# Kernel tuning notes

Hardware: AMD Instinct MI355X
Metric: run time of the kernel (lower is better)

Reference implementation:

```python
import jax, jax.numpy as jnp
import numpy as np

K = 1023   # kernel_size == embedding_dim
H = 16     # out_channels (filters per sample)
E = 256    # num_embeddings
T = 8      # num_tokens
CC = 0.25  # commitment cost
EPS = np.float32(np.finfo(np.float32).eps)
DN = ('NCH', 'OIH', 'NCH')


def setup_inputs() -> dict:
    key = jax.random.key(0)
    ks = jax.random.split(key, 10)
    B, C, L = 8, 1, 8184
    D_ff = 2 * E
    X = jax.random.normal(ks[0], (B, C, L), jnp.float32)
    embedding = jax.random.uniform(ks[1], (E, K), jnp.float32, -1.0 / E, 1.0 / E)
    ffn_w1 = jax.random.normal(ks[2], (E, D_ff), jnp.float32) * 0.02
    ffn_b1 = jnp.zeros((D_ff,), jnp.float32)
    ffn_w2 = jax.random.normal(ks[3], (D_ff, E), jnp.float32) * 0.02
    ffn_b2 = jnp.zeros((E,), jnp.float32)
    ln_g = jnp.ones((E,), jnp.float32)
    ln_b = jnp.zeros((E,), jnp.float32)
    cls_w = jax.random.normal(ks[4], (E, 10), jnp.float32) * 0.02
    cls_b = jnp.zeros((10,), jnp.float32)
    return dict(X=X, embedding=embedding, ffn_w1=ffn_w1, ffn_b1=ffn_b1,
                ffn_w2=ffn_w2, ffn_b2=ffn_b2, ln_g=ln_g, ln_b=ln_b,
                cls_w=cls_w, cls_b=cls_b)


def _autocov(f):
    # f: [..., K]. FFT-based autocovariance of hann-windowed, max-normalized frame.
    n = f.shape[-1]
    fmax = jnp.max(jnp.abs(f), axis=-1, keepdims=True)
    fmax = jnp.where(fmax == 0, EPS, fmax)
    win = 0.5 * (1.0 - jnp.cos(2.0 * jnp.pi * jnp.arange(n, dtype=jnp.float32) / n))
    xw = f * win / fmax
    spec = jnp.abs(jnp.fft.rfft(xw, n=n) ** 2)   # |rfft(x)^2| == |rfft(x)|^2
    return jnp.fft.ifftshift(jnp.fft.irfft(spec, n=n), axes=-1)


def reference(X, embedding, ffn_w1, ffn_b1, ffn_w2, ffn_b2, ln_g, ln_b, cls_w, cls_b):
    B, C, L = X.shape
    # ---- encoder: extract frames at fixed linspace positions, autocovariance ----
    Lp = ((L + K - 1) // K) * K          # PadForConv(zero) length (no-op here)
    end = Lp - K - 1 - K
    positions = jnp.linspace(0.0, float(end), H).astype(jnp.int32)
    idx = positions[:, None] + jnp.arange(K)          # (H, K)
    frames = X[:, :, idx]                             # (B, C, H, K) gather
    Z = _autocov(jnp.transpose(frames, (0, 2, 1, 3)))  # (B, H, C, K)
    # ---- VQ: pairwise distances + argmin + codebook lookup ----
    flat = Z.reshape(-1, K)                           # (B*H*C, K)
    d = (jnp.sum(flat ** 2, axis=1, keepdims=True)
         + jnp.sum(embedding ** 2, axis=1)
         - 2.0 * flat @ embedding.T)                  # (B*H*C, E)
    codes = jnp.argmin(d, axis=1)
    enc = jax.nn.one_hot(codes, E, dtype=flat.dtype)
    quant = (enc @ embedding).reshape(Z.shape)
    sg = jax.lax.stop_gradient
    e_loss = jnp.mean((sg(quant) - Z) ** 2)
    q_loss = jnp.mean((quant - sg(Z)) ** 2)
    vq_loss = q_loss + CC * e_loss
    quant_st = Z + sg(quant - Z)                      # straight-through
    avg = jnp.mean(enc, axis=0)
    perplexity = jnp.exp(-jnp.sum(avg * jnp.log(avg + EPS)))
    # ---- decoder: every sample's filter bank convolved with the whole batch ----
    fmerged = quant_st.reshape(B * H, C, K)           # merge per-sample banks
    out = jax.lax.conv_general_dilated(X, fmerged, (1,), 'SAME',
                                       dimension_numbers=DN)  # (B, B*H, L)
    out = out.reshape(B, B, H, L)                     # (batch b, filter-sample i, k, L)
    sq = (out - X[:, None, :, :]) ** 2                # C==1 broadcast
    # sum_i mean_k mse_{b,l} == mean over (b,k,l) then sum over i
    recon_loss = jnp.sum(jnp.mean(sq, axis=(0, 2, 3)))
    # ---- project: conv with codebook as filters ----
    pfilt = jnp.broadcast_to(embedding[:, None, :], (E, C, K))
    proj = jax.lax.conv_general_dilated(X, pfilt, (1,), 'VALID',
                                        dimension_numbers=DN)  # (B, E, Lo)
    Lo = proj.shape[-1]
    pad = ((Lo + T - 1) // T) * T - Lo                # PadForConv(mean)
    m = jnp.mean(proj, axis=-1, keepdims=True)
    proj = jnp.concatenate([proj, jnp.broadcast_to(m, (B, E, pad))], axis=-1)
    # ---- classify ----
    x = proj.reshape(B, E, T, -1).transpose(0, 2, 3, 1)  # (B, T, t, E)
    x = jnp.max(x, axis=2)                               # (B, T, E)
    mu = jnp.mean(x, axis=-1, keepdims=True)
    var = jnp.var(x, axis=-1, keepdims=True)
    xn = (x - mu) / jnp.sqrt(var + 1e-5) * ln_g + ln_b
    hdd = jax.nn.relu(xn @ ffn_w1 + ffn_b1) @ ffn_w2 + ffn_b2
    feat = jnp.mean(hdd, axis=1)                         # (B, E)
    logits = feat @ cls_w + cls_b
    return (logits, vq_loss, recon_loss, perplexity)
```

## Files before the change

### kernel.cpp

```cpp
#include <hip/hip_runtime.h>

#define KK 1023
#define LL 8184
#define LO 7162
#define XPS 10240
#define EPSF 1.1920928955078125e-07f
#define NEG_INF (-3.4028234663852886e+38f)

typedef short bf16x8 __attribute__((ext_vector_type(8)));
typedef float f32x4 __attribute__((ext_vector_type(4)));

__device__ __constant__ int c_pos[16] = {0,409,818,1227,1636,2045,2454,2863,
                                         3273,3682,4091,4500,4909,5318,5727,6137};

__device__ __forceinline__ unsigned short f2bf(float f) {
    unsigned u = __float_as_uint(f);
    unsigned r = (u + 0x7FFFu + ((u >> 16) & 1u)) >> 16;
    return (unsigned short)r;
}
__device__ __forceinline__ int fenc(float f) {
    int u = __float_as_int(f);
    return u >= 0 ? u : (~u) ^ 0x80000000;
}
__device__ __forceinline__ float fdec(int k) {
    int u = k >= 0 ? k : ~(k ^ 0x80000000);
    return __int_as_float(u);
}
__device__ __forceinline__ void gl2lds16(const void* g, void* l) {
    __builtin_amdgcn_global_load_lds(
        (const __attribute__((address_space(1))) void*)g,
        (__attribute__((address_space(3))) void*)l, 16, 0, 0);
}

__global__ __launch_bounds__(256) void k_pa(const float* __restrict__ X,
                                            const float* __restrict__ emb,
                                            unsigned short* __restrict__ Xpad,
                                            unsigned short* __restrict__ Xodd,
                                            unsigned short* __restrict__ Ebf,
                                            float* __restrict__ Etf,
                                            float* __restrict__ enorm,
                                            int* __restrict__ hist,
                                            int* __restrict__ cmax,
                                            float* __restrict__ Z) {
    __shared__ __align__(16) float xw[2048];
    __shared__ float red[256];
    const int q = blockIdx.x;
    const int tid = threadIdx.x;
    if (q < 256) {
        const int fi = q >> 1, half = q & 1;
        const int b = fi >> 4, h = fi & 15;
        const float* xp = X + b * LL + c_pos[h];
        float lmax = 0.f;
        for (int j = tid; j < KK; j += 256) {
            float v = xp[j];
            xw[j] = v;
            lmax = fmaxf(lmax, fabsf(v));
        }
        red[tid] = lmax;
        __syncthreads();
        for (int off = 128; off; off >>= 1) {
            if (tid < off) red[tid] = fmaxf(red[tid], red[tid + off]);
            __syncthreads();
        }
        float fmx = red[0];
        if (fmx == 0.f) fmx = EPSF;
        __syncthreads();
        for (int j = tid; j < KK; j += 256) {
            float v = xw[j];
            float win = 0.5f * (1.0f - cosf(6.28318530717958647692f * (float)j / 1023.0f));
            float w = v * win / fmx;
            xw[j] = w;
            xw[j + KK] = w;
        }
        __syncthreads();

        if (tid < 128) {
            const int m = half * 512 + 4 * tid;
            const int mh = m >> 1;
            const int mq4 = mh >> 1;
            const float2* X2 = (const float2*)xw;
            const float4* X4 = (const float4*)xw;
            float a0 = 0.f, a1 = 0.f, a2 = 0.f, a3 = 0.f;
            float2 W0 = X2[mh], W1 = X2[mh + 1], W2 = X2[mh + 2], W3 = X2[mh + 3];
            for (int jh = 0; jh < 510; jh += 2) {
                float4 nw = X4[mq4 + (jh >> 1) + 2];
                float4 xj = X4[jh >> 1];
                a0 = fmaf(xj.x, W0.x, a0);
                a0 = fmaf(xj.y, W0.y, a0);
                a0 = fmaf(xj.z, W1.x, a0);
                a0 = fmaf(xj.w, W1.y, a0);
                a1 = fmaf(xj.x, W0.y, a1);
                a1 = fmaf(xj.y, W1.x, a1);
                a1 = fmaf(xj.z, W1.y, a1);
                a1 = fmaf(xj.w, W2.x, a1);
                a2 = fmaf(xj.x, W1.x, a2);
                a2 = fmaf(xj.y, W1.y, a2);
                a2 = fmaf(xj.z, W2.x, a2);
                a2 = fmaf(xj.w, W2.y, a2);
                a3 = fmaf(xj.x, W1.y, a3);
                a3 = fmaf(xj.y, W2.x, a3);
                a3 = fmaf(xj.z, W2.y, a3);
                a3 = fmaf(xj.w, W3.x, a3);
                W0 = W2; W1 = W3;
                W2 = make_float2(nw.x, nw.y);
                W3 = make_float2(nw.z, nw.w);
            }
            {
                float2 xj = X2[510];
                a0 = fmaf(xj.x, W0.x, a0);
                a0 = fmaf(xj.y, W0.y, a0);
                a1 = fmaf(xj.x, W0.y, a1);
                a1 = fmaf(xj.y, W1.x, a1);
                a2 = fmaf(xj.x, W1.x, a2);
                a2 = fmaf(xj.y, W1.y, a2);
                a3 = fmaf(xj.x, W1.y, a3);
                a3 = fmaf(xj.y, W2.x, a3);
            }
            float xt = xw[1022];
            a0 = fmaf(xt, W1.x, a0);
            a1 = fmaf(xt, W1.y, a1);
            a2 = fmaf(xt, W2.x, a2);
            a3 = fmaf(xt, W2.y, a3);

            float* zrow = Z + fi * KK;
            float av[4] = {a0, a1, a2, a3};
#pragma unroll
            for (int qq = 0; qq < 4; ++qq) {
                int mmq = m + qq;
                if (mmq < KK) {
                    int i0 = mmq + 512; if (i0 >= KK) i0 -= KK;
                    zrow[i0] = av[qq];
                }
            }
        }
    } else if (q < 288) {
        const int qq = q - 256;
        const int b = qq >> 2, seg = qq & 3;
        for (int i = seg * 2560 + tid; i < (seg + 1) * 2560; i += 256) {
            unsigned short v = 0, vo = 0;
            if (i >= 512 && i < 512 + LL) v = f2bf(X[b * LL + (i - 512)]);
            const int i1 = i + 1;
            if (i1 >= 512 && i1 < 512 + LL) vo = f2bf(X[b * LL + (i1 - 512)]);
            Xpad[b * XPS + i] = v;
            Xodd[b * XPS + i] = vo;
        }
    } else if (q < 544) {
        const int e = q - 288;
        const float* er = emb + e * KK;
        float nrm = 0.f;
        for (int k = tid; k < 1024; k += 256) {
            float v = (k < KK) ? er[k] : 0.f;
            Ebf[e * 1024 + k] = (k < KK) ? f2bf(v) : (unsigned short)0;
            Etf[(k >> 2) * 1024 + e * 4 + (k & 3)] = v;
            nrm = fmaf(v, v, nrm);
        }
        red[tid] = nrm;
        __syncthreads();
        for (int off = 128; off; off >>= 1) {
            if (tid < off) red[tid] += red[tid + off];
            __syncthreads();
        }
        if (tid == 0) enorm[e] = red[0];
    } else {
        const int i = (q - 544) * 256 + tid;
        cmax[i] = INT_MIN;
        if (q == 544) hist[tid] = 0;
    }
}

__global__ __launch_bounds__(256) void k_vq(const float* __restrict__ Z,
                                            const float4* __restrict__ Et4,
                                            const float* __restrict__ enorm,
                                            const float* __restrict__ emb,
                                            int* __restrict__ codes,
                                            int* __restrict__ hist,
                                            float* __restrict__ vq_part) {
    __shared__ float zl[KK];
    __shared__ __align__(16) float zm2[1024];
    __shared__ float rv[256];
    __shared__ int   ri[256];
    const int fi = blockIdx.x, tid = threadIdx.x;
    const float* zrow = Z + fi * KK;
    for (int t = tid; t < 1024; t += 256) {
        float z = (t < KK) ? zrow[t] : 0.f;
        if (t < KK) zl[t] = z;
        zm2[t] = -2.f * z;
    }
    __syncthreads();

    float d = enorm[tid];
    const float4* zp = (const float4*)zm2;
    const float4* ep = Et4 + tid;
#pragma unroll 8
    for (int t4 = 0; t4 < 256; ++t4) {
        float4 ev = ep[t4 * 256];
        float4 zv = zp[t4];
        d = fmaf(zv.x, ev.x, d);
        d = fmaf(zv.y, ev.y, d);
        d = fmaf(zv.z, ev.z, d);
        d = fmaf(zv.w, ev.w, d);
    }
    rv[tid] = d; ri[tid] = tid;
    __syncthreads();
    for (int off = 128; off; off >>= 1) {
        if (tid < off) {
            float v2 = rv[tid + off]; int i2 = ri[tid + off];
            if (v2 < rv[tid] || (v2 == rv[tid] && i2 < ri[tid])) { rv[tid] = v2; ri[tid] = i2; }
        }
        __syncthreads();
    }
    const int code = ri[0];
    if (tid == 0) { codes[fi] = code; atomicAdd(&hist[code], 1); }

    const float* qr = emb + code * KK;
    float s = 0.f;
    for (int t = tid; t < KK; t += 256) { float dd = qr[t] - zl[t]; s += dd * dd; }
    __syncthreads();
    rv[tid] = s;
    __syncthreads();
    for (int off = 128; off; off >>= 1) {
        if (tid < off) rv[tid] += rv[tid + off];
        __syncthreads();
    }
    if (tid == 0) vq_part[fi] = rv[0];
}

__global__ __launch_bounds__(256, 4) void k_gemm(const unsigned short* __restrict__ Xpad,
                                                 const unsigned short* __restrict__ Xodd,
                                                 const unsigned short* __restrict__ Ebf,
                                                 const int* __restrict__ codes,
                                                 const float* __restrict__ X,
                                                 float* __restrict__ psum_part,
                                                 float* __restrict__ recon_part,
                                                 int* __restrict__ cmax) {
    __shared__ __align__(16) unsigned short lds_b[8 * 1280];
    __shared__ __align__(16) unsigned short lds_a[2 * 2048];
    __shared__ float red_s[64][4];
    const int tid  = threadIdx.x;
    const int lane = tid & 63;
    const int c = lane & 15, g = lane >> 4;
    const int wg = tid >> 6;

    const int bi = blockIdx.x;
    const bool isproj = bi < 896;
    int b, l0, row0;
    if (isproj) { b = bi / 112; int r = bi % 112; row0 = (r / 28) * 64; l0 = (r % 28) * 256; }
    else        { int q = bi - 896; b = q >> 6; int r = q & 63; row0 = (r >> 5) * 64; l0 = (r & 31) * 256; }
    const int xw0 = (isproj ? 512 : 0) + l0;

    {
        const unsigned short* base_e = Xpad + b * XPS + xw0;
        const unsigned short* base_o = Xodd + b * XPS + xw0;
        for (int k = tid; k < 1280; k += 256) {
            const int wdw = k / 160;
            const int p = k - wdw * 160;
            const unsigned short* src = (wdw & 1) ? (base_o + wdw - 1 + p * 8)
                                                  : (base_e + wdw + p * 8);
            gl2lds16(src, lds_b + k * 8);
        }
    }
    const int r_lds = tid >> 2, q4 = tid & 3;
    const int grow = isproj ? (row0 + r_lds) : codes[row0 + r_lds];
    const unsigned short* e_src = Ebf + grow * 1024 + q4 * 8;
    gl2lds16(e_src, lds_a + tid * 8);
    __syncthreads();

    f32x4 acc[4][4];
#pragma unroll
    for (int i = 0; i < 4; ++i)
#pragma unroll
        for (int j = 0; j < 4; ++j) acc[i][j] = (f32x4){0.f, 0.f, 0.f, 0.f};

    const char* lax = (const char*)lds_a;
    const char* lbx = (const char*)lds_b;
    const int boff0 = (wg & 1) * 10240 + ((wg >> 1) << 4) + 32 * c + 16 * g;
    const int aoff0 = c * 64 + g * 16;

    for (int s = 0; s < 32; ++s) {
        const int cur = s & 1;
        if (s + 1 < 32)
            gl2lds16(e_src + (s + 1) * 32, lds_a + ((s + 1) & 1) * 2048 + tid * 8);
        const char* ab = lax + cur * 4096 + aoff0;
        bf16x8 af[4];
#pragma unroll
        for (int et = 0; et < 4; ++et) af[et] = *(const bf16x8*)(ab + et * 1024);
#pragma unroll
        for (int ntl = 0; ntl < 4; ++ntl) {
            bf16x8 bfrag = *(const bf16x8*)(lbx + boff0 + ntl * 2560 + 64 * s);
#pragma unroll
            for (int et = 0; et < 4; ++et)
                acc[et][ntl] = __builtin_amdgcn_mfma_f32_16x16x32_bf16(af[et], bfrag, acc[et][ntl], 0, 0, 0);
        }
        __syncthreads();
    }

    const int lseg  = l0 >> 8;
    const int lbase = l0 + wg * 4;
    if (isproj) {
        const int ch0 = lbase / 896;
#pragma unroll
        for (int et = 0; et < 4; ++et) {
#pragma unroll
            for (int r = 0; r < 4; ++r) {
                float ssum = 0.f, m0 = NEG_INF, m1 = NEG_INF;
#pragma unroll
                for (int ntl = 0; ntl < 4; ++ntl) {
                    float v = acc[et][ntl][r];
                    int l = lbase + ntl + 16 * c;
                    bool ok = l < LO;
                    ssum += ok ? v : 0.f;
                    int ch = l / 896;
                    if (ok && ch == ch0) m0 = fmaxf(m0, v);
                    if (ok && ch != ch0) m1 = fmaxf(m1, v);
                }
                ssum += __shfl_xor(ssum, 1); ssum += __shfl_xor(ssum, 2);
                ssum += __shfl_xor(ssum, 4); ssum += __shfl_xor(ssum, 8);
                m0 = fmaxf(m0, __shfl_xor(m0, 1)); m0 = fmaxf(m0, __shfl_xor(m0, 2));
                m0 = fmaxf(m0, __shfl_xor(m0, 4)); m0 = fmaxf(m0, __shfl_xor(m0, 8));
                m1 = fmaxf(m1, __shfl_xor(m1, 1)); m1 = fmaxf(m1, __shfl_xor(m1, 2));
                m1 = fmaxf(m1, __shfl_xor(m1, 4)); m1 = fmaxf(m1, __shfl_xor(m1, 8));
                if (c == 0) {
                    int eidx = et * 16 + g * 4 + r;
                    red_s[eidx][wg] = ssum;
                    int e = row0 + eidx;
                    int cb = (b * 256 + e) * 8;
                    if (m0 > NEG_INF && ch0 < 8)     atomicMax(&cmax[cb + ch0], fenc(m0));
                    if (m1 > NEG_INF && ch0 + 1 < 8) atomicMax(&cmax[cb + ch0 + 1], fenc(m1));
                }
            }
        }
    } else {
        float xv[4];
#pragma unroll
        for (int ntl = 0; ntl < 4; ++ntl) {
            int lr = lbase + ntl + 16 * c - 1;
            xv[ntl] = (lr >= 0 && lr < LL) ? X[b * LL + lr] : 0.f;
        }
#pragma unroll
        for (int et = 0; et < 4; ++et) {
#pragma unroll
            for (int r = 0; r < 4; ++r) {
                float ssum = 0.f;
#pragma unroll
                for (int ntl = 0; ntl < 4; ++ntl) {
                    int lr = lbase + ntl + 16 * c - 1;
                    bool ok = (lr >= 0) && (lr < LL);
                    float dd = ok ? (acc[et][ntl][r] - xv[ntl]) : 0.f;
                    ssum += dd * dd;
                }
                ssum += __shfl_xor(ssum, 1); ssum += __shfl_xor(ssum, 2);
                ssum += __shfl_xor(ssum, 4); ssum += __shfl_xor(ssum, 8);
                if (c == 0) red_s[et * 16 + g * 4 + r][wg] = ssum;
            }
        }
    }
    __syncthreads();
    if (tid < 64) {
        float tot = red_s[tid][0] + red_s[tid][1] + red_s[tid][2] + red_s[tid][3];
        if (isproj) {
            int e = row0 + tid;
            psum_part[lseg * 2048 + b * 256 + e] = tot;
        } else {
            int f = row0 + tid;
            recon_part[(b * 128 + f) * 32 + lseg] = tot;
        }
    }
}

__global__ __launch_bounds__(256) void k_lnffn1(const float* __restrict__ psum_part,
                                                const int* __restrict__ cmax,
                                                const float* __restrict__ ln_g,
                                                const float* __restrict__ ln_b,
                                                const float* __restrict__ w1,
                                                const float* __restrict__ b1,
                                                float* __restrict__ hbuf) {
    __shared__ float red[256];
    __shared__ float red2[256];
    __shared__ float xr[256];
    const int bt = blockIdx.x;
    const int t = bt & 7;
    const int b = bt >> 3;
    const int e = threadIdx.x;
    const float* ps = psum_part + b * 256 + e;
    float sm = 0.f;
#pragma unroll
    for (int s = 0; s < 28; ++s) sm += ps[s * 2048];
    float m = sm * (1.0f / 7162.0f);
    const int cb = (b * 256 + e) << 3;
    float v = (t < 7) ? fdec(cmax[cb + t]) : fmaxf(fdec(cmax[cb + 7]), m);
    red[e] = v; red2[e] = v * v;
    __syncthreads();
    for (int off = 128; off; off >>= 1) {
        if (e < off) { red[e] += red[e + off]; red2[e] += red2[e + off]; }
        __syncthreads();
    }
    float mu  = red[0] * (1.0f / 256.0f);
    float var = red2[0] * (1.0f / 256.0f) - mu * mu;
    float r = 1.0f / sqrtf(var + 1e-5f);
    xr[e] = (v - mu) * r * ln_g[e] + ln_b[e];
    __syncthreads();

    float a0 = 0.f, a1 = 0.f;
#pragma unroll 4
    for (int ee = 0; ee < 256; ++ee) {
        float xv = xr[ee];
        a0 = fmaf(xv, w1[ee * 512 + e], a0);
        a1 = fmaf(xv, w1[ee * 512 + 256 + e], a1);
    }
    hbuf[bt * 512 + e]       = fmaxf(a0 + b1[e], 0.f);
    hbuf[bt * 512 + 256 + e] = fmaxf(a1 + b1[256 + e], 0.f);
}

__global__ __launch_bounds__(256) void k_ffn2(const float* __restrict__ hbuf,
                                              const float* __restrict__ w2,
                                              const float* __restrict__ b2,
                                              float* __restrict__ hdd) {
    __shared__ float hr[512];
    __shared__ float rv[256];
    const int q = blockIdx.x;
    const int bt = q & 63, jc = q >> 6;
    const int tid = threadIdx.x;
    hr[tid] = hbuf[bt * 512 + tid];
    hr[tid + 256] = hbuf[bt * 512 + 256 + tid];
    __syncthreads();
    const int jj = tid & 63, ks = tid >> 6;
    const int e = jc * 64 + jj;
    const float* wp = w2 + (ks * 128) * 256 + e;
    float a = 0.f;
#pragma unroll
    for (int j = 0; j < 128; ++j) a = fmaf(hr[ks * 128 + j], wp[j * 256], a);
    rv[tid] = a;
    __syncthreads();
    if (tid < 64) {
        float s = rv[tid] + rv[tid + 64] + rv[tid + 128] + rv[tid + 192];
        hdd[bt * 256 + jc * 64 + tid] = s + b2[jc * 64 + tid];
    }
}

__global__ __launch_bounds__(256) void k_final(const float* __restrict__ hdd,
                                               const float* __restrict__ cls_w,
                                               const float* __restrict__ cls_b,
                                               const float* __restrict__ recon_part,
                                               const float* __restrict__ vq_part,
                                               const int* __restrict__ hist,
                                               float* __restrict__ out) {
    __shared__ float red[256];
    const int tid = threadIdx.x;
    if (blockIdx.x == 0) {
        __shared__ float feat[8][256];
#pragma unroll
        for (int b2 = 0; b2 < 8; ++b2) {
            float fb = 0.f;
#pragma unroll
            for (int t2 = 0; t2 < 8; ++t2) fb += hdd[(b2 * 8 + t2) * 256 + tid];
            feat[b2][tid] = fb * 0.125f;
        }
        __syncthreads();
        if (tid < 80) {
            const int b = tid / 10, k = tid % 10;
            float a = cls_b[k];
            for (int e = 0; e < 256; ++e) a = fmaf(feat[b][e], cls_w[e * 10 + k], a);
            out[tid] = a;
        }
    } else {
        float s = 0.f;
        for (int i = tid; i < 32768; i += 256) s += recon_part[i];
        red[tid] = s;
        __syncthreads();
        for (int off = 128; off; off >>= 1) { if (tid < off) red[tid] += red[tid + off]; __syncthreads(); }
        if (tid == 0) out[81] = red[0] / 1047552.0f;
        __syncthreads();
        red[tid] = (tid < 128) ? vq_part[tid] : 0.f;
        __syncthreads();
        for (int off = 128; off; off >>= 1) { if (tid < off) red[tid] += red[tid + off]; __syncthreads(); }
        if (tid == 0) out[80] = 1.25f * red[0] / 130944.0f;
        __syncthreads();
        float avg = (float)hist[tid] * (1.0f / 128.0f);
        red[tid] = avg * logf(avg + EPSF);
        __syncthreads();
        for (int off = 128; off; off >>= 1) { if (tid < off) red[tid] += red[tid + off]; __syncthreads(); }
        if (tid == 0) out[82] = expf(-red[0]);
    }
}

extern "C" void kernel_launch(void* const* d_in, const int* in_sizes, int n_in,
                              void* d_out, int out_size, void* d_ws, size_t ws_size,
                              hipStream_t stream) {
    const float* X     = (const float*)d_in[0];
    const float* emb   = (const float*)d_in[1];
    const float* w1    = (const float*)d_in[2];
    const float* b1    = (const float*)d_in[3];
    const float* w2    = (const float*)d_in[4];
    const float* b2    = (const float*)d_in[5];
    const float* ln_g  = (const float*)d_in[6];
    const float* ln_b  = (const float*)d_in[7];
    const float* cls_w = (const float*)d_in[8];
    const float* cls_b = (const float*)d_in[9];
    float* out = (float*)d_out;

    float* Z            = (float*)d_ws;
    float* vq_part      = Z + 130944;
    float* xnbuf        = vq_part + 128;
    float* hdd          = xnbuf + 16384;
    float* psum_part    = hdd + 16384;
    float* recon_part   = psum_part + 65536;
    int*   cmaxb        = (int*)(recon_part + 32768);
    int*   codes        = cmaxb + 16384;
    int*   hist         = codes + 128;
    unsigned short* Xpad = (unsigned short*)(hist + 256);
    unsigned short* Xodd = Xpad + 8 * XPS;
    unsigned short* Ebf  = Xodd + 8 * XPS;
    float* Etf           = (float*)(Ebf + 256 * 1024);
    float* enorm         = Etf + 256 * 1024;
    float* hbuf          = enorm + 256;

    k_pa     <<<dim3(608), dim3(256), 0, stream>>>(X, emb, Xpad, Xodd, Ebf, Etf, enorm, hist, cmaxb, Z);
    k_vq     <<<dim3(128), dim3(256), 0, stream>>>(Z, (const float4*)Etf, enorm, emb, codes, hist, vq_part);
    k_gemm   <<<dim3(1408), dim3(256), 0, stream>>>(Xpad, Xodd, Ebf, codes, X, psum_part, recon_part, cmaxb);
    k_lnffn1 <<<dim3(64),  dim3(256), 0, stream>>>(psum_part, cmaxb, ln_g, ln_b, w1, b1, hbuf);
    k_ffn2   <<<dim3(256), dim3(256), 0, stream>>>(hbuf, w2, b2, hdd);
    k_final  <<<dim3(2),   dim3(256), 0, stream>>>(hdd, cls_w, cls_b, recon_part, vq_part, hist, out);
}
```

Before: 139.9 us.

## Restructure kernel graph to overlap independent stages in merged launches

The VQ kernel is merged with the projection GEMM blocks, and the LayerNorm/FFN1 stage is merged with the reconstruction GEMM blocks. FFN2 is merged with the loss reductions, and the classifier becomes its own tiny kernel. Each launch now runs independent work side by side, which cuts serial dependency depth and fills idle CUs with small tail stages. The cost is shared-memory union sizing and branch-divergent block roles that may change occupancy.

```diff
diff --git a/kernel.cpp b/kernel.cpp
--- a/kernel.cpp
+++ b/kernel.cpp
@@ -168,85 +168,85 @@
     }
 }
 
-__global__ __launch_bounds__(256) void k_vq(const float* __restrict__ Z,
-                                            const float4* __restrict__ Et4,
-                                            const float* __restrict__ enorm,
-                                            const float* __restrict__ emb,
-                                            int* __restrict__ codes,
-                                            int* __restrict__ hist,
-                                            float* __restrict__ vq_part) {
-    __shared__ float zl[KK];
-    __shared__ __align__(16) float zm2[1024];
-    __shared__ float rv[256];
-    __shared__ int   ri[256];
-    const int fi = blockIdx.x, tid = threadIdx.x;
-    const float* zrow = Z + fi * KK;
-    for (int t = tid; t < 1024; t += 256) {
-        float z = (t < KK) ? zrow[t] : 0.f;
-        if (t < KK) zl[t] = z;
-        zm2[t] = -2.f * z;
-    }
-    __syncthreads();
-
-    float d = enorm[tid];
-    const float4* zp = (const float4*)zm2;
-    const float4* ep = Et4 + tid;
+__global__ __launch_bounds__(256, 4) void kA(const float* __restrict__ Z,
+                                             const float4* __restrict__ Et4,
+                                             const float* __restrict__ enorm,
+                                             const float* __restrict__ emb,
+                                             int* __restrict__ codes,
+                                             int* __restrict__ hist,
+                                             float* __restrict__ vq_part,
+                                             const unsigned short* __restrict__ Xpad,
+                                             const unsigned short* __restrict__ Xodd,
+                                             const unsigned short* __restrict__ Ebf,
+                                             float* __restrict__ psum_part,
+                                             int* __restrict__ cmax) {
+    __shared__ __align__(16) char smem[29696];
+    const int tid = threadIdx.x;
+    const int bi = blockIdx.x;
+    if (bi < 128) {
+        float* zl  = (float*)smem;
+        float* zm2 = (float*)(smem + 4096);
+        float* rv  = (float*)(smem + 8192);
+        int*   ri  = (int*)(smem + 9216);
+        const int fi = bi;
+        const float* zrow = Z + fi * KK;
+        for (int t = tid; t < 1024; t += 256) {
+            float z = (t < KK) ? zrow[t] : 0.f;
+            if (t < KK) zl[t] = z;
+            zm2[t] = -2.f * z;
+        }
+        __syncthreads();
+
+        float d = enorm[tid];
+        const float4* zp = (const float4*)zm2;
+        const float4* ep = Et4 + tid;
 #pragma unroll 8
-    for (int t4 = 0; t4 < 256; ++t4) {
-        float4 ev = ep[t4 * 256];
-        float4 zv = zp[t4];
-        d = fmaf(zv.x, ev.x, d);
-        d = fmaf(zv.y, ev.y, d);
-        d = fmaf(zv.z, ev.z, d);
-        d = fmaf(zv.w, ev.w, d);
-    }
-    rv[tid] = d; ri[tid] = tid;
-    __syncthreads();
-    for (int off = 128; off; off >>= 1) {
-        if (tid < off) {
-            float v2 = rv[tid + off]; int i2 = ri[tid + off];
-            if (v2 < rv[tid] || (v2 == rv[tid] && i2 < ri[tid])) { rv[tid] = v2; ri[tid] = i2; }
-        }
-        __syncthreads();
-    }
-    const int code = ri[0];
-    if (tid == 0) { codes[fi] = code; atomicAdd(&hist[code], 1); }
-
-    const float* qr = emb + code * KK;
-    float s = 0.f;
-    for (int t = tid; t < KK; t += 256) { float dd = qr[t] - zl[t]; s += dd * dd; }
-    __syncthreads();
-    rv[tid] = s;
-    __syncthreads();
-    for (int off = 128; off; off >>= 1) {
-        if (tid < off) rv[tid] += rv[tid + off];
-        __syncthreads();
-    }
-    if (tid == 0) vq_part[fi] = rv[0];
-}
-
-__global__ __launch_bounds__(256, 4) void k_gemm(const unsigned short* __restrict__ Xpad,
-                                                 const unsigned short* __restrict__ Xodd,
-                                                 const unsigned short* __restrict__ Ebf,
-                                                 const int* __restrict__ codes,
-                                                 const float* __restrict__ X,
-                                                 float* __restrict__ psum_part,
-                                                 float* __restrict__ recon_part,
-                                                 int* __restrict__ cmax) {
-    __shared__ __align__(16) unsigned short lds_b[8 * 1280];
-    __shared__ __align__(16) unsigned short lds_a[2 * 2048];
-    __shared__ float red_s[64][4];
-    const int tid  = threadIdx.x;
+        for (int t4 = 0; t4 < 256; ++t4) {
+            float4 ev = ep[t4 * 256];
+            float4 zv = zp[t4];
+            d = fmaf(zv.x, ev.x, d);
+            d = fmaf(zv.y, ev.y, d);
+            d = fmaf(zv.z, ev.z, d);
+            d = fmaf(zv.w, ev.w, d);
+        }
+        rv[tid] = d; ri[tid] = tid;
+        __syncthreads();
+        for (int off = 128; off; off >>= 1) {
+            if (tid < off) {
+                float v2 = rv[tid + off]; int i2 = ri[tid + off];
+                if (v2 < rv[tid] || (v2 == rv[tid] && i2 < ri[tid])) { rv[tid] = v2; ri[tid] = i2; }
+            }
+            __syncthreads();
+        }
+        const int code = ri[0];
+        if (tid == 0) { codes[fi] = code; atomicAdd(&hist[code], 1); }
+
+        const float* qr = emb + code * KK;
+        float s = 0.f;
+        for (int t = tid; t < KK; t += 256) { float dd = qr[t] - zl[t]; s += dd * dd; }
+        __syncthreads();
+        rv[tid] = s;
+        __syncthreads();
+        for (int off = 128; off; off >>= 1) {
+            if (tid < off) rv[tid] += rv[tid + off];
+            __syncthreads();
+        }
+        if (tid == 0) vq_part[fi] = rv[0];
+        return;
+    }
+    unsigned short* lds_b = (unsigned short*)smem;
+    unsigned short* lds_a = (unsigned short*)(smem + 20480);
+    float (*red_s)[4] = (float(*)[4])(smem + 28672);
     const int lane = tid & 63;
     const int c = lane & 15, g = lane >> 4;
     const int wg = tid >> 6;
 
-    const int bi = blockIdx.x;
-    const bool isproj = bi < 896;
-    int b, l0, row0;
-    if (isproj) { b = bi / 112; int r = bi % 112; row0 = (r / 28) * 64; l0 = (r % 28) * 256; }
-    else        { int q = bi - 896; b = q >> 6; int r = q & 63; row0 = (r >> 5) * 64; l0 = (r & 31) * 256; }
-    const int xw0 = (isproj ? 512 : 0) + l0;
+    const int pb = bi - 128;
+    const int b = pb / 112;
+    const int r = pb % 112;
+    const int row0 = (r / 28) * 64;
+    const int l0 = (r % 28) * 256;
+    const int xw0 = 512 + l0;
 
     {
         const unsigned short* base_e = Xpad + b * XPS + xw0;
@@ -260,8 +260,7 @@
         }
     }
     const int r_lds = tid >> 2, q4 = tid & 3;
-    const int grow = isproj ? (row0 + r_lds) : codes[row0 + r_lds];
-    const unsigned short* e_src = Ebf + grow * 1024 + q4 * 8;
+    const unsigned short* e_src = Ebf + (row0 + r_lds) * 1024 + q4 * 8;
     gl2lds16(e_src, lds_a + tid * 8);
     __syncthreads();
 
@@ -296,173 +295,222 @@
 
     const int lseg  = l0 >> 8;
     const int lbase = l0 + wg * 4;
-    if (isproj) {
-        const int ch0 = lbase / 896;
-#pragma unroll
-        for (int et = 0; et < 4; ++et) {
-#pragma unroll
-            for (int r = 0; r < 4; ++r) {
-                float ssum = 0.f, m0 = NEG_INF, m1 = NEG_INF;
-#pragma unroll
-                for (int ntl = 0; ntl < 4; ++ntl) {
-                    float v = acc[et][ntl][r];
-                    int l = lbase + ntl + 16 * c;
-                    bool ok = l < LO;
-                    ssum += ok ? v : 0.f;
-                    int ch = l / 896;
-                    if (ok && ch == ch0) m0 = fmaxf(m0, v);
-                    if (ok && ch != ch0) m1 = fmaxf(m1, v);
-                }
-                ssum += __shfl_xor(ssum, 1); ssum += __shfl_xor(ssum, 2);
-                ssum += __shfl_xor(ssum, 4); ssum += __shfl_xor(ssum, 8);
-                m0 = fmaxf(m0, __shfl_xor(m0, 1)); m0 = fmaxf(m0, __shfl_xor(m0, 2));
-                m0 = fmaxf(m0, __shfl_xor(m0, 4)); m0 = fmaxf(m0, __shfl_xor(m0, 8));
-                m1 = fmaxf(m1, __shfl_xor(m1, 1)); m1 = fmaxf(m1, __shfl_xor(m1, 2));
-                m1 = fmaxf(m1, __shfl_xor(m1, 4)); m1 = fmaxf(m1, __shfl_xor(m1, 8));
-                if (c == 0) {
-                    int eidx = et * 16 + g * 4 + r;
-                    red_s[eidx][wg] = ssum;
-                    int e = row0 + eidx;
-                    int cb = (b * 256 + e) * 8;
-                    if (m0 > NEG_INF && ch0 < 8)     atomicMax(&cmax[cb + ch0], fenc(m0));
-                    if (m1 > NEG_INF && ch0 + 1 < 8) atomicMax(&cmax[cb + ch0 + 1], fenc(m1));
-                }
-            }
-        }
-    } else {
-        float xv[4];
-#pragma unroll
-        for (int ntl = 0; ntl < 4; ++ntl) {
-            int lr = lbase + ntl + 16 * c - 1;
-            xv[ntl] = (lr >= 0 && lr < LL) ? X[b * LL + lr] : 0.f;
-        }
-#pragma unroll
-        for (int et = 0; et < 4; ++et) {
-#pragma unroll
-            for (int r = 0; r < 4; ++r) {
-                float ssum = 0.f;
-#pragma unroll
-                for (int ntl = 0; ntl < 4; ++ntl) {
-                    int lr = lbase + ntl + 16 * c - 1;
-                    bool ok = (lr >= 0) && (lr < LL);
-                    float dd = ok ? (acc[et][ntl][r] - xv[ntl]) : 0.f;
-                    ssum += dd * dd;
-                }
-                ssum += __shfl_xor(ssum, 1); ssum += __shfl_xor(ssum, 2);
-                ssum += __shfl_xor(ssum, 4); ssum += __shfl_xor(ssum, 8);
-                if (c == 0) red_s[et * 16 + g * 4 + r][wg] = ssum;
+    const int ch0 = lbase / 896;
+#pragma unroll
+    for (int et = 0; et < 4; ++et) {
+#pragma unroll
+        for (int r4 = 0; r4 < 4; ++r4) {
+            float ssum = 0.f, m0 = NEG_INF, m1 = NEG_INF;
+#pragma unroll
+            for (int ntl = 0; ntl < 4; ++ntl) {
+                float v = acc[et][ntl][r4];
+                int l = lbase + ntl + 16 * c;
+                bool ok = l < LO;
+                ssum += ok ? v : 0.f;
+                int ch = l / 896;
+                if (ok && ch == ch0) m0 = fmaxf(m0, v);
+                if (ok && ch != ch0) m1 = fmaxf(m1, v);
+            }
+            ssum += __shfl_xor(ssum, 1); ssum += __shfl_xor(ssum, 2);
+            ssum += __shfl_xor(ssum, 4); ssum += __shfl_xor(ssum, 8);
+            m0 = fmaxf(m0, __shfl_xor(m0, 1)); m0 = fmaxf(m0, __shfl_xor(m0, 2));
+            m0 = fmaxf(m0, __shfl_xor(m0, 4)); m0 = fmaxf(m0, __shfl_xor(m0, 8));
+            m1 = fmaxf(m1, __shfl_xor(m1, 1)); m1 = fmaxf(m1, __shfl_xor(m1, 2));
+            m1 = fmaxf(m1, __shfl_xor(m1, 4)); m1 = fmaxf(m1, __shfl_xor(m1, 8));
+            if (c == 0) {
+                int eidx = et * 16 + g * 4 + r4;
+                red_s[eidx][wg] = ssum;
+                int e = row0 + eidx;
+                int cb = (b * 256 + e) * 8;
+                if (m0 > NEG_INF && ch0 < 8)     atomicMax(&cmax[cb + ch0], fenc(m0));
+                if (m1 > NEG_INF && ch0 + 1 < 8) atomicMax(&cmax[cb + ch0 + 1], fenc(m1));
             }
         }
     }
     __syncthreads();
     if (tid < 64) {
         float tot = red_s[tid][0] + red_s[tid][1] + red_s[tid][2] + red_s[tid][3];
-        if (isproj) {
-            int e = row0 + tid;
-            psum_part[lseg * 2048 + b * 256 + e] = tot;
-        } else {
-            int f = row0 + tid;
-            recon_part[(b * 128 + f) * 32 + lseg] = tot;
-        }
-    }
-}
-
-__global__ __launch_bounds__(256) void k_lnffn1(const float* __restrict__ psum_part,
-                                                const int* __restrict__ cmax,
-                                                const float* __restrict__ ln_g,
-                                                const float* __restrict__ ln_b,
-                                                const float* __restrict__ w1,
-                                                const float* __restrict__ b1,
-                                                float* __restrict__ hbuf) {
-    __shared__ float red[256];
-    __shared__ float red2[256];
-    __shared__ float xr[256];
-    const int bt = blockIdx.x;
-    const int t = bt & 7;
-    const int b = bt >> 3;
-    const int e = threadIdx.x;
-    const float* ps = psum_part + b * 256 + e;
-    float sm = 0.f;
-#pragma unroll
-    for (int s = 0; s < 28; ++s) sm += ps[s * 2048];
-    float m = sm * (1.0f / 7162.0f);
-    const int cb = (b * 256 + e) << 3;
-    float v = (t < 7) ? fdec(cmax[cb + t]) : fmaxf(fdec(cmax[cb + 7]), m);
-    red[e] = v; red2[e] = v * v;
+        psum_part[lseg * 2048 + b * 256 + row0 + tid] = tot;
+    }
+}
+
+__global__ __launch_bounds__(256, 4) void kB(const float* __restrict__ psum_part,
+                                             const int* __restrict__ cmax,
+                                             const float* __restrict__ ln_g,
+                                             const float* __restrict__ ln_b,
+                                             const float* __restrict__ w1,
+                                             const float* __restrict__ b1,
+                                             float* __restrict__ hbuf,
+                                             const unsigned short* __restrict__ Xpad,
+                                             const unsigned short* __restrict__ Xodd,
+                                             const unsigned short* __restrict__ Ebf,
+                                             const int* __restrict__ codes,
+                                             const float* __restrict__ X,
+                                             float* __restrict__ recon_part) {
+    __shared__ __align__(16) char smem[29696];
+    const int tid = threadIdx.x;
+    const int bi = blockIdx.x;
+    if (bi < 64) {
+        float* red  = (float*)smem;
+        float* red2 = (float*)(smem + 1024);
+        float* xr   = (float*)(smem + 2048);
+        const int bt = bi;
+        const int t = bt & 7;
+        const int b = bt >> 3;
+        const int e = tid;
+        const float* ps = psum_part + b * 256 + e;
+        float sm = 0.f;
+#pragma unroll
+        for (int s = 0; s < 28; ++s) sm += ps[s * 2048];
+        float m = sm * (1.0f / 7162.0f);
+        const int cb = (b * 256 + e) << 3;
+        float v = (t < 7) ? fdec(cmax[cb + t]) : fmaxf(fdec(cmax[cb + 7]), m);
+        red[e] = v; red2[e] = v * v;
+        __syncthreads();
+        for (int off = 128; off; off >>= 1) {
+            if (e < off) { red[e] += red[e + off]; red2[e] += red2[e + off]; }
+            __syncthreads();
+        }
+        float mu  = red[0] * (1.0f / 256.0f);
+        float var = red2[0] * (1.0f / 256.0f) - mu * mu;
+        float rr = 1.0f / sqrtf(var + 1e-5f);
+        xr[e] = (v - mu) * rr * ln_g[e] + ln_b[e];
+        __syncthreads();
+
+        float a0 = 0.f, a1 = 0.f;
+#pragma unroll 4
+        for (int ee = 0; ee < 256; ++ee) {
+            float xv = xr[ee];
+            a0 = fmaf(xv, w1[ee * 512 + e], a0);
+            a1 = fmaf(xv, w1[ee * 512 + 256 + e], a1);
+        }
+        hbuf[bt * 512 + e]       = fmaxf(a0 + b1[e], 0.f);
+        hbuf[bt * 512 + 256 + e] = fmaxf(a1 + b1[256 + e], 0.f);
+        return;
+    }
+    unsigned short* lds_b = (unsigned short*)smem;
+    unsigned short* lds_a = (unsigned short*)(smem + 20480);
+    float (*red_s)[4] = (float(*)[4])(smem + 28672);
+    const int lane = tid & 63;
+    const int c = lane & 15, g = lane >> 4;
+    const int wg = tid >> 6;
+
+    const int rb = bi - 64;
+    const int b = rb >> 6;
+    const int r = rb & 63;
+    const int row0 = (r >> 5) * 64;
+    const int l0 = (r & 31) * 256;
+    const int xw0 = l0;
+
+    {
+        const unsigned short* base_e = Xpad + b * XPS + xw0;
+        const unsigned short* base_o = Xodd + b * XPS + xw0;
+        for (int k = tid; k < 1280; k += 256) {
+            const int wdw = k / 160;
+            const int p = k - wdw * 160;
+            const unsigned short* src = (wdw & 1) ? (base_o + wdw - 1 + p * 8)
+                                                  : (base_e + wdw + p * 8);
+            gl2lds16(src, lds_b + k * 8);
+        }
+    }
+    const int r_lds = tid >> 2, q4 = tid & 3;
+    const unsigned short* e_src = Ebf + codes[row0 + r_lds] * 1024 + q4 * 8;
+    gl2lds16(e_src, lds_a + tid * 8);
     __syncthreads();
-    for (int off = 128; off; off >>= 1) {
-        if (e < off) { red[e] += red[e + off]; red2[e] += red2[e + off]; }
-        __syncthreads();
-    }
-    float mu  = red[0] * (1.0f / 256.0f);
-    float var = red2[0] * (1.0f / 256.0f) - mu * mu;
-    float r = 1.0f / sqrtf(var + 1e-5f);
-    xr[e] = (v - mu) * r * ln_g[e] + ln_b[e];
-    __syncthreads();
-
-    float a0 = 0.f, a1 = 0.f;
-#pragma unroll 4
-    for (int ee = 0; ee < 256; ++ee) {
-        float xv = xr[ee];
-        a0 = fmaf(xv, w1[ee * 512 + e], a0);
-        a1 = fmaf(xv, w1[ee * 512 + 256 + e], a1);
-    }
-    hbuf[bt * 512 + e]       = fmaxf(a0 + b1[e], 0.f);
-    hbuf[bt * 512 + 256 + e] = fmaxf(a1 + b1[256 + e], 0.f);
-}
-
-__global__ __launch_bounds__(256) void k_ffn2(const float* __restrict__ hbuf,
-                                              const float* __restrict__ w2,
-                                              const float* __restrict__ b2,
-                                              float* __restrict__ hdd) {
-    __shared__ float hr[512];
-    __shared__ float rv[256];
-    const int q = blockIdx.x;
-    const int bt = q & 63, jc = q >> 6;
-    const int tid = threadIdx.x;
-    hr[tid] = hbuf[bt * 512 + tid];
-    hr[tid + 256] = hbuf[bt * 512 + 256 + tid];
-    __syncthreads();
-    const int jj = tid & 63, ks = tid >> 6;
-    const int e = jc * 64 + jj;
-    const float* wp = w2 + (ks * 128) * 256 + e;
-    float a = 0.f;
-#pragma unroll
-    for (int j = 0; j < 128; ++j) a = fmaf(hr[ks * 128 + j], wp[j * 256], a);
-    rv[tid] = a;
+
+    f32x4 acc[4][4];
+#pragma unroll
+    for (int i = 0; i < 4; ++i)
+#pragma unroll
+        for (int j = 0; j < 4; ++j) acc[i][j] = (f32x4){0.f, 0.f, 0.f, 0.f};
+
+    const char* lax = (const char*)lds_a;
+    const char* lbx = (const char*)lds_b;
+    const int boff0 = (wg & 1) * 10240 + ((wg >> 1) << 4) + 32 * c + 16 * g;
+    const int aoff0 = c * 64 + g * 16;
+
+    for (int s = 0; s < 32; ++s) {
+        const int cur = s & 1;
+        if (s + 1 < 32)
+            gl2lds16(e_src + (s + 1) * 32, lds_a + ((s + 1) & 1) * 2048 + tid * 8);
+        const char* ab = lax + cur * 4096 + aoff0;
+        bf16x8 af[4];
+#pragma unroll
+        for (int et = 0; et < 4; ++et) af[et] = *(const bf16x8*)(ab + et * 1024);
+#pragma unroll
+        for (int ntl = 0; ntl < 4; ++ntl) {
+            bf16x8 bfrag = *(const bf16x8*)(lbx + boff0 + ntl * 2560 + 64 * s);
+#pragma unroll
+            for (int et = 0; et < 4; ++et)
+                acc[et][ntl] = __builtin_amdgcn_mfma_f32_16x16x32_bf16(af[et], bfrag, acc[et][ntl], 0, 0, 0);
+        }
+        __syncthreads();
+    }
+
+    const int lseg  = l0 >> 8;
+    const int lbase = l0 + wg * 4;
+    float xv[4];
+#pragma unroll
+    for (int ntl = 0; ntl < 4; ++ntl) {
+        int lr = lbase + ntl + 16 * c - 1;
+        xv[ntl] = (lr >= 0 && lr < LL) ? X[b * LL + lr] : 0.f;
+    }
+#pragma unroll
+    for (int et = 0; et < 4; ++et) {
+#pragma unroll
+        for (int r4 = 0; r4 < 4; ++r4) {
+            float ssum = 0.f;
+#pragma unroll
+            for (int ntl = 0; ntl < 4; ++ntl) {
+                int lr = lbase + ntl + 16 * c - 1;
+                bool ok = (lr >= 0) && (lr < LL);
+                float dd = ok ? (acc[et][ntl][r4] - xv[ntl]) : 0.f;
+                ssum += dd * dd;
+            }
+            ssum += __shfl_xor(ssum, 1); ssum += __shfl_xor(ssum, 2);
+            ssum += __shfl_xor(ssum, 4); ssum += __shfl_xor(ssum, 8);
+            if (c == 0) red_s[et * 16 + g * 4 + r4][wg] = ssum;
+        }
+    }
     __syncthreads();
     if (tid < 64) {
-        float s = rv[tid] + rv[tid + 64] + rv[tid + 128] + rv[tid + 192];
-        hdd[bt * 256 + jc * 64 + tid] = s + b2[jc * 64 + tid];
-    }
-}
-
-__global__ __launch_bounds__(256) void k_final(const float* __restrict__ hdd,
-                                               const float* __restrict__ cls_w,
-                                               const float* __restrict__ cls_b,
-                                               const float* __restrict__ recon_part,
-                                               const float* __restrict__ vq_part,
-                                               const int* __restrict__ hist,
-                                               float* __restrict__ out) {
-    __shared__ float red[256];
+        float tot = red_s[tid][0] + red_s[tid][1] + red_s[tid][2] + red_s[tid][3];
+        recon_part[(b * 128 + row0 + tid) * 32 + lseg] = tot;
+    }
+}
+
+__global__ __launch_bounds__(256) void kC(const float* __restrict__ hbuf,
+                                          const float* __restrict__ w2,
+                                          const float* __restrict__ b2,
+                                          float* __restrict__ hdd,
+                                          const float* __restrict__ recon_part,
+                                          const float* __restrict__ vq_part,
+                                          const int* __restrict__ hist,
+                                          float* __restrict__ out) {
+    __shared__ __align__(16) char smem[3072];
     const int tid = threadIdx.x;
-    if (blockIdx.x == 0) {
-        __shared__ float feat[8][256];
-#pragma unroll
-        for (int b2 = 0; b2 < 8; ++b2) {
-            float fb = 0.f;
-#pragma unroll
-            for (int t2 = 0; t2 < 8; ++t2) fb += hdd[(b2 * 8 + t2) * 256 + tid];
-            feat[b2][tid] = fb * 0.125f;
-        }
-        __syncthreads();
-        if (tid < 80) {
-            const int b = tid / 10, k = tid % 10;
-            float a = cls_b[k];
-            for (int e = 0; e < 256; ++e) a = fmaf(feat[b][e], cls_w[e * 10 + k], a);
-            out[tid] = a;
+    const int bi = blockIdx.x;
+    if (bi < 256) {
+        float* hr = (float*)smem;
+        float* rv = (float*)(smem + 2048);
+        const int bt = bi & 63, jc = bi >> 6;
+        hr[tid] = hbuf[bt * 512 + tid];
+        hr[tid + 256] = hbuf[bt * 512 + 256 + tid];
+        __syncthreads();
+        const int jj = tid & 63, ks = tid >> 6;
+        const int e = jc * 64 + jj;
+        const float* wp = w2 + (ks * 128) * 256 + e;
+        float a = 0.f;
+#pragma unroll
+        for (int j = 0; j < 128; ++j) a = fmaf(hr[ks * 128 + j], wp[j * 256], a);
+        rv[tid] = a;
+        __syncthreads();
+        if (tid < 64) {
+            float s = rv[tid] + rv[tid + 64] + rv[tid + 128] + rv[tid + 192];
+            hdd[bt * 256 + jc * 64 + tid] = s + b2[jc * 64 + tid];
         }
     } else {
+        float* red = (float*)smem;
         float s = 0.f;
         for (int i = tid; i < 32768; i += 256) s += recon_part[i];
         red[tid] = s;
@@ -480,6 +528,28 @@
         __syncthreads();
         for (int off = 128; off; off >>= 1) { if (tid < off) red[tid] += red[tid + off]; __syncthreads(); }
         if (tid == 0) out[82] = expf(-red[0]);
+    }
+}
+
+__global__ __launch_bounds__(256) void kD(const float* __restrict__ hdd,
+                                          const float* __restrict__ cls_w,
+                                          const float* __restrict__ cls_b,
+                                          float* __restrict__ out) {
+    __shared__ float feat[8][256];
+    const int tid = threadIdx.x;
+#pragma unroll
+    for (int b2 = 0; b2 < 8; ++b2) {
+        float fb = 0.f;
+#pragma unroll
+        for (int t2 = 0; t2 < 8; ++t2) fb += hdd[(b2 * 8 + t2) * 256 + tid];
+        feat[b2][tid] = fb * 0.125f;
+    }
+    __syncthreads();
+    if (tid < 80) {
+        const int b = tid / 10, k = tid % 10;
+        float a = cls_b[k];
+        for (int e = 0; e < 256; ++e) a = fmaf(feat[b][e], cls_w[e * 10 + k], a);
+        out[tid] = a;
     }
 }
 
@@ -514,10 +584,11 @@
     float* enorm         = Etf + 256 * 1024;
     float* hbuf          = enorm + 256;
 
-    k_pa     <<<dim3(608), dim3(256), 0, stream>>>(X, emb, Xpad, Xodd, Ebf, Etf, enorm, hist, cmaxb, Z);
-    k_vq     <<<dim3(128), dim3(256), 0, stream>>>(Z, (const float4*)Etf, enorm, emb, codes, hist, vq_part);
-    k_gemm   <<<dim3(1408), dim3(256), 0, stream>>>(Xpad, Xodd, Ebf, codes, X, psum_part, recon_part, cmaxb);
-    k_lnffn1 <<<dim3(64),  dim3(256), 0, stream>>>(psum_part, cmaxb, ln_g, ln_b, w1, b1, hbuf);
-    k_ffn2   <<<dim3(256), dim3(256), 0, stream>>>(hbuf, w2, b2, hdd);
-    k_final  <<<dim3(2),   dim3(256), 0, stream>>>(hdd, cls_w, cls_b, recon_part, vq_part, hist, out);
-}
+    k_pa<<<dim3(608), dim3(256), 0, stream>>>(X, emb, Xpad, Xodd, Ebf, Etf, enorm, hist, cmaxb, Z);
+    kA  <<<dim3(1024), dim3(256), 0, stream>>>(Z, (const float4*)Etf, enorm, emb, codes, hist,
+                                               vq_part, Xpad, Xodd, Ebf, psum_part, cmaxb);
+    kB  <<<dim3(576), dim3(256), 0, stream>>>(psum_part, cmaxb, ln_g, ln_b, w1, b1, hbuf,
+                                              Xpad, Xodd, Ebf, codes, X, recon_part);
+    kC  <<<dim3(257), dim3(256), 0, stream>>>(hbuf, w2, b2, hdd, recon_part, vq_part, hist, out);
+    kD  <<<dim3(1),   dim3(256), 0, stream>>>(hdd, cls_w, cls_b, out);
+}
```

Result: faster. 122.4 us (-12.5%).
